# Optimization experiments

Measured on AMD Instinct MI355X. Metric: run time of the kernel, lower is better.

The kernel has to match this reference:

```python
import jax, jax.numpy as jnp
import numpy as np

C = 256      # MSA_channels
PC = 256     # pair_channels
G = 4        # groups
GP = C // G  # group_planes
FF = 4 * C
EPS = 1e-5


def layernorm(x, w, b):
    mu = jnp.mean(x, axis=-1, keepdims=True)
    var = jnp.mean(jnp.square(x - mu), axis=-1, keepdims=True)
    return (x - mu) * jax.lax.rsqrt(var + EPS) * w + b


def setup_inputs() -> dict:
    key = jax.random.key(0)
    ks = jax.random.split(key, 12)
    N, D, L = 1, 64, 512
    s = lambda fan_in: 1.0 / np.sqrt(fan_in)
    return {
        "msa_matrix": jax.random.normal(ks[0], (N, D, L, C), jnp.float32),
        "rr_edge": jax.random.normal(ks[1], (N, L, L, PC), jnp.float32),
        "ln_msa_w": jnp.ones((C,), jnp.float32),
        "ln_msa_b": jnp.zeros((C,), jnp.float32),
        "ln_rr_w": jnp.ones((PC,), jnp.float32),
        "ln_rr_b": jnp.zeros((PC,), jnp.float32),
        "WA": jax.random.normal(ks[2], (PC, G), jnp.float32) * s(PC),
        "bA": jnp.zeros((G,), jnp.float32),
        "WV": jax.random.normal(ks[3], (C, C), jnp.float32) * s(C),
        "bV": jnp.zeros((C,), jnp.float32),
        "WO": jax.random.normal(ks[4], (C, C), jnp.float32) * s(C),
        "bO": jnp.zeros((C,), jnp.float32),
        "ln_ff_w": jnp.ones((C,), jnp.float32),
        "ln_ff_b": jnp.zeros((C,), jnp.float32),
        "W1": jax.random.normal(ks[5], (C, FF), jnp.float32) * s(C),
        "b1": jnp.zeros((FF,), jnp.float32),
        "W2": jax.random.normal(ks[6], (FF, C), jnp.float32) * s(FF),
        "b2": jnp.zeros((C,), jnp.float32),
    }


def reference(msa_matrix, rr_edge, ln_msa_w, ln_msa_b, ln_rr_w, ln_rr_b,
              WA, bA, WV, bV, WO, bO, ln_ff_w, ln_ff_b, W1, b1, W2, b2):
    N, D, L, _ = msa_matrix.shape
    raw = msa_matrix
    m = layernorm(msa_matrix, ln_msa_w, ln_msa_b)          # [N,D,L,C]
    E = 0.5 * (rr_edge + jnp.swapaxes(rr_edge, 1, 2))      # symmetrize [N,L,L,PC]
    E = layernorm(E, ln_rr_w, ln_rr_b)
    A = jax.nn.softmax(E @ WA + bA, axis=2)                # [N,L,L,G], softmax over key dim j
    V = (m @ WV + bV).reshape(N, D, L, G, GP)              # [N,D,L,G,GP]
    agg = jnp.einsum('nijg,ndjgc->ndigc', A, V).reshape(N, D, L, C)
    out = agg @ WO + bO
    x = raw + out                                          # residual (dropout = identity at eval)
    h = layernorm(x, ln_ff_w, ln_ff_b)                     # FFN with pre-LN + residual
    return x + (jax.nn.relu(h @ W1 + b1) @ W2 + b2)
```

## Files before the change

### kernel.cpp

```cpp
#include <hip/hip_runtime.h>
#include <hip/hip_bf16.h>

typedef __bf16 bf16;
typedef bf16 bf16x8 __attribute__((ext_vector_type(8)));
typedef bf16 bf16x4v __attribute__((ext_vector_type(4)));
typedef float f32x4 __attribute__((ext_vector_type(4)));

#define LN_EPS 1e-5f

__device__ __forceinline__ void gload_lds16(const bf16* gsrc, bf16* ldst) {
  __builtin_amdgcn_global_load_lds(
      (const __attribute__((address_space(1))) void*)gsrc,
      (__attribute__((address_space(3))) void*)ldst, 16, 0, 0);
}

__global__ __launch_bounds__(256) void ln_rows_kernel(
    const float* __restrict__ in, const float* __restrict__ w,
    const float* __restrict__ b, bf16* __restrict__ out)
{
  int row = blockIdx.x * 4 + (threadIdx.x >> 6);
  int lane = threadIdx.x & 63;
  const float4* p = (const float4*)(in + (size_t)row * 256);
  float4 v = p[lane];
  float s = v.x + v.y + v.z + v.w;
  float q = v.x*v.x + v.y*v.y + v.z*v.z + v.w*v.w;
  #pragma unroll
  for (int o = 32; o; o >>= 1) { s += __shfl_xor(s, o); q += __shfl_xor(q, o); }
  float mu = s * (1.0f/256.0f);
  float rs = rsqrtf(q*(1.0f/256.0f) - mu*mu + LN_EPS);
  float4 wv = ((const float4*)w)[lane];
  float4 bv = ((const float4*)b)[lane];
  bf16x4v o4;
  o4[0] = (bf16)((v.x - mu)*rs*wv.x + bv.x);
  o4[1] = (bf16)((v.y - mu)*rs*wv.y + bv.y);
  o4[2] = (bf16)((v.z - mu)*rs*wv.z + bv.z);
  o4[3] = (bf16)((v.w - mu)*rs*wv.w + bv.w);
  *(bf16x4v*)(out + (size_t)row * 256 + lane * 4) = o4;
}

__global__ __launch_bounds__(256) void transpose_all_kernel(
    const float* __restrict__ WV, const float* __restrict__ WO,
    const float* __restrict__ W1, const float* __restrict__ W2,
    bf16* __restrict__ WVt, bf16* __restrict__ WOt,
    bf16* __restrict__ W1t, bf16* __restrict__ W2t)
{
  __shared__ float tile[32][33];
  int id = blockIdx.x;
  const float* in; bf16* out; int R, C, tpr;
  if (id < 64)       { in = WV; out = WVt; R = 256;  C = 256;  tpr = 8;  }
  else if (id < 128) { in = WO; out = WOt; R = 256;  C = 256;  tpr = 8;  id -= 64; }
  else if (id < 384) { in = W1; out = W1t; R = 256;  C = 1024; tpr = 32; id -= 128; }
  else               { in = W2; out = W2t; R = 1024; C = 256;  tpr = 8;  id -= 384; }
  int bc = (id % tpr) * 32, br = (id / tpr) * 32;
  int tx = threadIdx.x, ty = threadIdx.y;
  #pragma unroll
  for (int i = ty; i < 32; i += 8)
    tile[i][tx] = in[(size_t)(br + i) * C + bc + tx];
  __syncthreads();
  #pragma unroll
  for (int i = ty; i < 32; i += 8)
    out[(size_t)(bc + i) * R + br + tx] = (bf16)tile[tx][i];
}

__global__ __launch_bounds__(256) void sym_ln_wa_kernel(
    const float* __restrict__ rr, const float* __restrict__ w,
    const float* __restrict__ b, const float* __restrict__ WA,
    float* __restrict__ S)
{
  int rem = blockIdx.x; int ti = 0; int len = 32;
  while (rem >= len) { rem -= len; ti++; len--; }
  int tj = ti + rem;
  int wid = threadIdx.x >> 6, lane = threadIdx.x & 63;
  int c0 = lane * 4;
  float4 wv = ((const float4*)w)[lane];
  float4 bv = ((const float4*)b)[lane];
  const float4* wa4 = (const float4*)WA;
  float4 wa0 = wa4[c0+0], wa1 = wa4[c0+1], wa2 = wa4[c0+2], wa3 = wa4[c0+3];
  int pend = blockIdx.y * 64 + 64;
  for (int p = blockIdx.y * 64 + wid; p < pend; p += 4) {
    int i = ti*16 + (p >> 4), j = tj*16 + (p & 15);
    float4 a = ((const float4*)(rr + ((size_t)i*512 + j)*256))[lane];
    float4 c = ((const float4*)(rr + ((size_t)j*512 + i)*256))[lane];
    float ex = 0.5f*(a.x + c.x), ey = 0.5f*(a.y + c.y),
          ez = 0.5f*(a.z + c.z), ew = 0.5f*(a.w + c.w);
    float s = ex+ey+ez+ew;
    float q = ex*ex+ey*ey+ez*ez+ew*ew;
    #pragma unroll
    for (int o = 32; o; o >>= 1) { s += __shfl_xor(s, o); q += __shfl_xor(q, o); }
    float mu = s*(1.f/256.f);
    float rs = rsqrtf(q*(1.f/256.f) - mu*mu + LN_EPS);
    float nx = (ex-mu)*rs*wv.x + bv.x;
    float ny = (ey-mu)*rs*wv.y + bv.y;
    float nz = (ez-mu)*rs*wv.z + bv.z;
    float nw = (ew-mu)*rs*wv.w + bv.w;
    float g0 = nx*wa0.x + ny*wa1.x + nz*wa2.x + nw*wa3.x;
    float g1 = nx*wa0.y + ny*wa1.y + nz*wa2.y + nw*wa3.y;
    float g2 = nx*wa0.z + ny*wa1.z + nz*wa2.z + nw*wa3.z;
    float g3 = nx*wa0.w + ny*wa1.w + nz*wa2.w + nw*wa3.w;
    #pragma unroll
    for (int o = 32; o; o >>= 1) {
      g0 += __shfl_xor(g0, o); g1 += __shfl_xor(g1, o);
      g2 += __shfl_xor(g2, o); g3 += __shfl_xor(g3, o);
    }
    if (lane == 0) {
      float4 r4 = make_float4(g0, g1, g2, g3);
      ((float4*)S)[(size_t)i*512 + j] = r4;
      ((float4*)S)[(size_t)j*512 + i] = r4;
    }
  }
}

__global__ __launch_bounds__(256) void softmax_kernel(
    const float* __restrict__ S, bf16* __restrict__ Aout)
{
  int i = blockIdx.x * 4 + (threadIdx.x >> 6);
  int lane = threadIdx.x & 63;
  const float4* Sr = (const float4*)S + (size_t)i * 512;
  float4 s[8];
  float m0 = -1e30f, m1 = -1e30f, m2 = -1e30f, m3 = -1e30f;
  #pragma unroll
  for (int it = 0; it < 8; it++) {
    s[it] = Sr[lane + it*64];
    m0 = fmaxf(m0, s[it].x); m1 = fmaxf(m1, s[it].y);
    m2 = fmaxf(m2, s[it].z); m3 = fmaxf(m3, s[it].w);
  }
  #pragma unroll
  for (int o = 32; o; o >>= 1) {
    m0 = fmaxf(m0, __shfl_xor(m0, o)); m1 = fmaxf(m1, __shfl_xor(m1, o));
    m2 = fmaxf(m2, __shfl_xor(m2, o)); m3 = fmaxf(m3, __shfl_xor(m3, o));
  }
  float t0=0.f, t1=0.f, t2=0.f, t3=0.f;
  #pragma unroll
  for (int it = 0; it < 8; it++) {
    s[it].x = __expf(s[it].x - m0); t0 += s[it].x;
    s[it].y = __expf(s[it].y - m1); t1 += s[it].y;
    s[it].z = __expf(s[it].z - m2); t2 += s[it].z;
    s[it].w = __expf(s[it].w - m3); t3 += s[it].w;
  }
  #pragma unroll
  for (int o = 32; o; o >>= 1) {
    t0 += __shfl_xor(t0, o); t1 += __shfl_xor(t1, o);
    t2 += __shfl_xor(t2, o); t3 += __shfl_xor(t3, o);
  }
  t0 = 1.f/t0; t1 = 1.f/t1; t2 = 1.f/t2; t3 = 1.f/t3;
  bf16* A0 = Aout + (size_t)i * 512;
  #pragma unroll
  for (int it = 0; it < 8; it++) {
    int j = lane + it*64;
    A0[j]          = (bf16)(s[it].x * t0);
    A0[262144 + j] = (bf16)(s[it].y * t1);
    A0[524288 + j] = (bf16)(s[it].z * t2);
    A0[786432 + j] = (bf16)(s[it].w * t3);
  }
}

template<int MODE>
__global__ __launch_bounds__(256) void gemm_bt_kernel(
    const bf16* __restrict__ Aglob, const bf16* __restrict__ Bglob,
    void* __restrict__ outP, const float* __restrict__ bias,
    const float* __restrict__ resid, int M, int N, int K)
{
  __shared__ bf16 As[2][128 * 32];
  __shared__ bf16 Bs[2][128 * 32];
  int g = blockIdx.z;
  const bf16* Ag = Aglob;
  const bf16* Bg = Bglob;
  if (MODE == 1) { Ag += (size_t)g * 512 * 512; Bg += (size_t)g * 4096 * 512; }
  int bm = blockIdx.y * 128, bn = blockIdx.x * 128;
  int tid = threadIdx.x;
  int wid = tid >> 6, lane = tid & 63;
  int wm = (wid >> 1) * 64, wn = (wid & 1) * 64;
  f32x4 acc[4][4];
  #pragma unroll
  for (int mi = 0; mi < 4; mi++)
    #pragma unroll
    for (int ni = 0; ni < 4; ni++)
      acc[mi][ni] = (f32x4){0.f, 0.f, 0.f, 0.f};
  int c0 = wid * 2, c1 = wid * 2 + 1;
  int srow = lane >> 2;
  int scol = (lane & 3) * 8;
  const bf16* a0 = &Ag[(size_t)(bm + c0*16 + srow) * K + scol];
  const bf16* a1 = &Ag[(size_t)(bm + c1*16 + srow) * K + scol];
  const bf16* b0 = &Bg[(size_t)(bn + c0*16 + srow) * K + scol];
  const bf16* b1 = &Bg[(size_t)(bn + c1*16 + srow) * K + scol];
  int fr = lane & 15, fk = (lane >> 4) * 8;
  int nt = K >> 5;
  gload_lds16(a0, &As[0][c0 * 512]);
  gload_lds16(a1, &As[0][c1 * 512]);
  gload_lds16(b0, &Bs[0][c0 * 512]);
  gload_lds16(b1, &Bs[0][c1 * 512]);
  int cur = 0;
  for (int t = 0; t < nt; t++) {
    if (t + 1 < nt) {
      int k1 = (t + 1) << 5;
      gload_lds16(a0 + k1, &As[cur ^ 1][c0 * 512]);
      gload_lds16(a1 + k1, &As[cur ^ 1][c1 * 512]);
      gload_lds16(b0 + k1, &Bs[cur ^ 1][c0 * 512]);
      gload_lds16(b1 + k1, &Bs[cur ^ 1][c1 * 512]);
      asm volatile("s_waitcnt vmcnt(4)" ::: "memory");
    } else {
      asm volatile("s_waitcnt vmcnt(0)" ::: "memory");
    }
    __builtin_amdgcn_s_barrier();
    __builtin_amdgcn_sched_barrier(0);
    bf16x8 af[4], bf_[4];
    #pragma unroll
    for (int mi = 0; mi < 4; mi++) af[mi] = *(const bf16x8*)&As[cur][(wm + mi*16 + fr) * 32 + fk];
    #pragma unroll
    for (int ni = 0; ni < 4; ni++) bf_[ni] = *(const bf16x8*)&Bs[cur][(wn + ni*16 + fr) * 32 + fk];
    #pragma unroll
    for (int mi = 0; mi < 4; mi++)
      #pragma unroll
      for (int ni = 0; ni < 4; ni++)
        acc[mi][ni] = __builtin_amdgcn_mfma_f32_16x16x32_bf16(af[mi], bf_[ni], acc[mi][ni], 0, 0, 0);
    __builtin_amdgcn_sched_barrier(0);
    __builtin_amdgcn_s_barrier();
    cur ^= 1;
  }
  int cn0 = lane & 15;
  int rq = (lane >> 4) * 4;
  #pragma unroll
  for (int mi = 0; mi < 4; mi++) {
    #pragma unroll
    for (int ni = 0; ni < 4; ni++) {
      int mb = bm + wm + mi*16 + rq;
      int nc = bn + wn + ni*16 + cn0;
      #pragma unroll
      for (int r = 0; r < 4; r++) {
        int mr = mb + r;
        float v = acc[mi][ni][r];
        if (MODE == 0) {
          v += bias[mr];
          int gg = mr >> 6, rp = mr & 63, d = nc >> 9, j = nc & 511;
          ((bf16*)outP)[((size_t)gg*4096 + d*64 + rp)*512 + j] = (bf16)v;
        } else if (MODE == 1) {
          int d = nc >> 6, c6 = nc & 63;
          ((bf16*)outP)[((size_t)d*512 + mr)*256 + g*64 + c6] = (bf16)v;
        } else {
          v += bias[nc] + resid[(size_t)mr * N + nc];
          ((float*)outP)[(size_t)mr * N + nc] = v;
        }
      }
    }
  }
}

__global__ __launch_bounds__(256) void ffn_fused_kernel(
    const float* __restrict__ x, const float* __restrict__ lnw,
    const float* __restrict__ lnb, const bf16* __restrict__ W1t,
    const float* __restrict__ b1, const bf16* __restrict__ W2t,
    const float* __restrict__ b2, float* __restrict__ out)
{
  __shared__ __align__(16) char hbuf[64 * 512];
  __shared__ __align__(16) char tbuf[64 * 512];
  int tid = threadIdx.x;
  int wid = tid >> 6, lane = tid & 63;
  size_t row0 = (size_t)blockIdx.x * 64;

  {
    float4 wv = ((const float4*)lnw)[lane];
    float4 bv = ((const float4*)lnb)[lane];
    #pragma unroll 4
    for (int it = 0; it < 16; it++) {
      int row = wid * 16 + it;
      float4 v = ((const float4*)(x + (row0 + row) * 256))[lane];
      float s = v.x+v.y+v.z+v.w, q = v.x*v.x+v.y*v.y+v.z*v.z+v.w*v.w;
      #pragma unroll
      for (int o = 32; o; o >>= 1) { s += __shfl_xor(s, o); q += __shfl_xor(q, o); }
      float mu = s * (1.f/256.f);
      float rs = rsqrtf(q*(1.f/256.f) - mu*mu + LN_EPS);
      bf16x4v o4;
      o4[0] = (bf16)((v.x-mu)*rs*wv.x + bv.x);
      o4[1] = (bf16)((v.y-mu)*rs*wv.y + bv.y);
      o4[2] = (bf16)((v.z-mu)*rs*wv.z + bv.z);
      o4[3] = (bf16)((v.w-mu)*rs*wv.w + bv.w);
      *(bf16x4v*)(hbuf + row*512 + ((lane*8) ^ ((row & 7) << 4))) = o4;
    }
  }
  __syncthreads();

  int wn = wid * 64;
  int fr = lane & 15;
  int fk = (lane >> 4) * 8;
  int fk2 = fk * 2;
  int cn0 = lane & 15, rq = (lane >> 4) * 4;
  int arow[4], asw[4], brow[4];
  #pragma unroll
  for (int mi = 0; mi < 4; mi++) {
    arow[mi] = mi*16 + fr;
    asw[mi]  = (arow[mi] & 7) << 4;
  }
  #pragma unroll
  for (int ni = 0; ni < 4; ni++) brow[ni] = wn + ni*16 + fr;

  f32x4 acc2[4][4];
  #pragma unroll
  for (int mi = 0; mi < 4; mi++)
    #pragma unroll
    for (int ni = 0; ni < 4; ni++)
      acc2[mi][ni] = (f32x4){0.f, 0.f, 0.f, 0.f};

  for (int cf = 0; cf < 4; cf++) {
    f32x4 acc1[4][4];
    #pragma unroll
    for (int mi = 0; mi < 4; mi++)
      #pragma unroll
      for (int ni = 0; ni < 4; ni++)
        acc1[mi][ni] = (f32x4){0.f, 0.f, 0.f, 0.f};
    #pragma unroll 2
    for (int k0 = 0; k0 < 256; k0 += 32) {
      bf16x8 af[4], bf_[4];
      #pragma unroll
      for (int ni = 0; ni < 4; ni++)
        bf_[ni] = *(const bf16x8*)&W1t[(size_t)(cf*256 + brow[ni]) * 256 + k0 + fk];
      #pragma unroll
      for (int mi = 0; mi < 4; mi++)
        af[mi] = *(const bf16x8*)(hbuf + arow[mi]*512 + ((k0*2 + fk2) ^ asw[mi]));
      #pragma unroll
      for (int mi = 0; mi < 4; mi++)
        #pragma unroll
        for (int ni = 0; ni < 4; ni++)
          acc1[mi][ni] = __builtin_amdgcn_mfma_f32_16x16x32_bf16(af[mi], bf_[ni], acc1[mi][ni], 0, 0, 0);
    }
    __syncthreads();
    #pragma unroll
    for (int ni = 0; ni < 4; ni++) {
      int col = wn + ni*16 + cn0;
      float bb = b1[cf*256 + col];
      #pragma unroll
      for (int mi = 0; mi < 4; mi++) {
        #pragma unroll
        for (int r = 0; r < 4; r++) {
          int row = mi*16 + rq + r;
          float v = fmaxf(acc1[mi][ni][r] + bb, 0.f);
          *(bf16*)(tbuf + row*512 + ((col*2) ^ ((row & 7) << 4))) = (bf16)v;
        }
      }
    }
    __syncthreads();
    #pragma unroll 2
    for (int k0 = 0; k0 < 256; k0 += 32) {
      bf16x8 af[4], bf_[4];
      #pragma unroll
      for (int ni = 0; ni < 4; ni++)
        bf_[ni] = *(const bf16x8*)&W2t[(size_t)brow[ni] * 1024 + cf*256 + k0 + fk];
      #pragma unroll
      for (int mi = 0; mi < 4; mi++)
        af[mi] = *(const bf16x8*)(tbuf + arow[mi]*512 + ((k0*2 + fk2) ^ asw[mi]));
      #pragma unroll
      for (int mi = 0; mi < 4; mi++)
        #pragma unroll
        for (int ni = 0; ni < 4; ni++)
          acc2[mi][ni] = __builtin_amdgcn_mfma_f32_16x16x32_bf16(af[mi], bf_[ni], acc2[mi][ni], 0, 0, 0);
    }
  }
  #pragma unroll
  for (int ni = 0; ni < 4; ni++) {
    int col = wn + ni*16 + cn0;
    float bb = b2[col];
    #pragma unroll
    for (int mi = 0; mi < 4; mi++) {
      #pragma unroll
      for (int r = 0; r < 4; r++) {
        size_t grow = row0 + mi*16 + rq + r;
        out[grow*256 + col] = x[grow*256 + col] + acc2[mi][ni][r] + bb;
      }
    }
  }
}

extern "C" void kernel_launch(void* const* d_in, const int* in_sizes, int n_in,
                              void* d_out, int out_size, void* d_ws, size_t ws_size,
                              hipStream_t stream)
{
  (void)in_sizes; (void)n_in; (void)out_size; (void)ws_size;
  const float* msa = (const float*)d_in[0];
  const float* rr  = (const float*)d_in[1];
  const float* lmw = (const float*)d_in[2];
  const float* lmb = (const float*)d_in[3];
  const float* lrw = (const float*)d_in[4];
  const float* lrb = (const float*)d_in[5];
  const float* WA  = (const float*)d_in[6];
  const float* WV  = (const float*)d_in[8];
  const float* bV  = (const float*)d_in[9];
  const float* WO  = (const float*)d_in[10];
  const float* bO  = (const float*)d_in[11];
  const float* lfw = (const float*)d_in[12];
  const float* lfb = (const float*)d_in[13];
  const float* W1  = (const float*)d_in[14];
  const float* b1  = (const float*)d_in[15];
  const float* W2  = (const float*)d_in[16];
  const float* b2  = (const float*)d_in[17];
  float* out = (float*)d_out;
  char* ws = (char*)d_ws;
  float* S    = (float*)(ws + 0);
  bf16* Abuf  = (bf16*)(ws + 4194304);
  bf16* m     = (bf16*)(ws + 6291456);
  bf16* Vt    = (bf16*)(ws + 23068672);
  bf16* agg   = (bf16*)(ws + 39845888);
  bf16* WVt   = (bf16*)(ws + 83886080);
  bf16* WOt   = WVt + 65536;
  bf16* W1t   = WOt + 65536;
  bf16* W2t   = W1t + 262144;

  transpose_all_kernel<<<640, dim3(32, 8), 0, stream>>>(WV, WO, W1, W2, WVt, WOt, W1t, W2t);

  ln_rows_kernel<<<8192, 256, 0, stream>>>(msa, lmw, lmb, m);
  sym_ln_wa_kernel<<<dim3(528, 4), 256, 0, stream>>>(rr, lrw, lrb, WA, S);
  gemm_bt_kernel<0><<<dim3(256, 2, 1), 256, 0, stream>>>(WVt, m, Vt, bV, nullptr, 256, 32768, 256);
  softmax_kernel<<<128, 256, 0, stream>>>(S, Abuf);
  gemm_bt_kernel<1><<<dim3(32, 4, 4), 256, 0, stream>>>(Abuf, Vt, agg, nullptr, nullptr, 512, 4096, 512);
  gemm_bt_kernel<2><<<dim3(2, 256, 1), 256, 0, stream>>>(agg, WOt, out, bO, msa, 32768, 256, 256);
  ffn_fused_kernel<<<512, 256, 0, stream>>>(out, lfw, lfb, W1t, b1, W2t, b2, out);
}
```

Baseline: 263.0 us.

## Split fused FFN into LN+GEMM1 kernel and separate GEMM2 via workspace

Replaces the single fused FFN kernel, which kept the hidden activation in LDS and read weights straight from global memory, with two kernels. The first does the layernorm plus the first matmul with ReLU on 128x128 tiles, double-buffering W1 in LDS through direct global-to-LDS loads, and writes the bf16 hidden tensor to workspace. The existing tiled GEMM then computes the second matmul with bias and residual. This is meant to raise MFMA utilisation and weight reuse, at the cost of a 64 MB hidden-tensor round trip through HBM. Each first-stage block also recomputes the layernorm for its rows, so it is repeated once per column tile.

```diff
diff --git a/kernel.cpp b/kernel.cpp
--- a/kernel.cpp
+++ b/kernel.cpp
@@ -245,25 +245,23 @@
   }
 }
 
-__global__ __launch_bounds__(256) void ffn_fused_kernel(
+__global__ __launch_bounds__(256) void ffn1_kernel(
     const float* __restrict__ x, const float* __restrict__ lnw,
     const float* __restrict__ lnb, const bf16* __restrict__ W1t,
-    const float* __restrict__ b1, const bf16* __restrict__ W2t,
-    const float* __restrict__ b2, float* __restrict__ out)
-{
-  __shared__ __align__(16) char hbuf[64 * 512];
-  __shared__ __align__(16) char tbuf[64 * 512];
+    const float* __restrict__ b1, bf16* __restrict__ tout)
+{
+  __shared__ __align__(16) char hbuf[128 * 512];
+  __shared__ bf16 Bs[2][128 * 32];
   int tid = threadIdx.x;
   int wid = tid >> 6, lane = tid & 63;
-  size_t row0 = (size_t)blockIdx.x * 64;
+  int bm = blockIdx.y * 128, bn = blockIdx.x * 128;
 
   {
     float4 wv = ((const float4*)lnw)[lane];
     float4 bv = ((const float4*)lnb)[lane];
-    #pragma unroll 4
-    for (int it = 0; it < 16; it++) {
-      int row = wid * 16 + it;
-      float4 v = ((const float4*)(x + (row0 + row) * 256))[lane];
+    for (int it = 0; it < 32; it++) {
+      int row = wid * 32 + it;
+      float4 v = ((const float4*)(x + (size_t)(bm + row) * 256))[lane];
       float s = v.x+v.y+v.z+v.w, q = v.x*v.x+v.y*v.y+v.z*v.z+v.w*v.w;
       #pragma unroll
       for (int o = 32; o; o >>= 1) { s += __shfl_xor(s, o); q += __shfl_xor(q, o); }
@@ -279,91 +277,70 @@
   }
   __syncthreads();
 
-  int wn = wid * 64;
-  int fr = lane & 15;
-  int fk = (lane >> 4) * 8;
-  int fk2 = fk * 2;
-  int cn0 = lane & 15, rq = (lane >> 4) * 4;
-  int arow[4], asw[4], brow[4];
+  int wm = (wid >> 1) * 64, wn = (wid & 1) * 64;
+  int fr = lane & 15, fk = (lane >> 4) * 8, fk2 = fk * 2;
+  int arow[4], asw[4];
   #pragma unroll
   for (int mi = 0; mi < 4; mi++) {
-    arow[mi] = mi*16 + fr;
+    arow[mi] = wm + mi*16 + fr;
     asw[mi]  = (arow[mi] & 7) << 4;
   }
-  #pragma unroll
-  for (int ni = 0; ni < 4; ni++) brow[ni] = wn + ni*16 + fr;
-
-  f32x4 acc2[4][4];
+  f32x4 acc[4][4];
   #pragma unroll
   for (int mi = 0; mi < 4; mi++)
     #pragma unroll
     for (int ni = 0; ni < 4; ni++)
-      acc2[mi][ni] = (f32x4){0.f, 0.f, 0.f, 0.f};
-
-  for (int cf = 0; cf < 4; cf++) {
-    f32x4 acc1[4][4];
+      acc[mi][ni] = (f32x4){0.f, 0.f, 0.f, 0.f};
+
+  int c0 = wid * 2, c1 = wid * 2 + 1;
+  int srow = lane >> 2;
+  int scol = (lane & 3) * 8;
+  const bf16* b0 = &W1t[(size_t)(bn + c0*16 + srow) * 256 + scol];
+  const bf16* b1p = &W1t[(size_t)(bn + c1*16 + srow) * 256 + scol];
+  gload_lds16(b0, &Bs[0][c0 * 512]);
+  gload_lds16(b1p, &Bs[0][c1 * 512]);
+  int cur = 0;
+  for (int t = 0; t < 8; t++) {
+    if (t < 7) {
+      int k1 = (t + 1) << 5;
+      gload_lds16(b0 + k1, &Bs[cur ^ 1][c0 * 512]);
+      gload_lds16(b1p + k1, &Bs[cur ^ 1][c1 * 512]);
+      asm volatile("s_waitcnt vmcnt(2)" ::: "memory");
+    } else {
+      asm volatile("s_waitcnt vmcnt(0)" ::: "memory");
+    }
+    __builtin_amdgcn_s_barrier();
+    __builtin_amdgcn_sched_barrier(0);
+    int k0 = t << 5;
+    bf16x8 af[4], bf_[4];
     #pragma unroll
     for (int mi = 0; mi < 4; mi++)
+      af[mi] = *(const bf16x8*)(hbuf + arow[mi]*512 + ((k0*2 + fk2) ^ asw[mi]));
+    #pragma unroll
+    for (int ni = 0; ni < 4; ni++)
+      bf_[ni] = *(const bf16x8*)&Bs[cur][(wn + ni*16 + fr) * 32 + fk];
+    #pragma unroll
+    for (int mi = 0; mi < 4; mi++)
       #pragma unroll
       for (int ni = 0; ni < 4; ni++)
-        acc1[mi][ni] = (f32x4){0.f, 0.f, 0.f, 0.f};
-    #pragma unroll 2
-    for (int k0 = 0; k0 < 256; k0 += 32) {
-      bf16x8 af[4], bf_[4];
-      #pragma unroll
-      for (int ni = 0; ni < 4; ni++)
-        bf_[ni] = *(const bf16x8*)&W1t[(size_t)(cf*256 + brow[ni]) * 256 + k0 + fk];
-      #pragma unroll
-      for (int mi = 0; mi < 4; mi++)
-        af[mi] = *(const bf16x8*)(hbuf + arow[mi]*512 + ((k0*2 + fk2) ^ asw[mi]));
-      #pragma unroll
-      for (int mi = 0; mi < 4; mi++)
-        #pragma unroll
-        for (int ni = 0; ni < 4; ni++)
-          acc1[mi][ni] = __builtin_amdgcn_mfma_f32_16x16x32_bf16(af[mi], bf_[ni], acc1[mi][ni], 0, 0, 0);
-    }
-    __syncthreads();
-    #pragma unroll
-    for (int ni = 0; ni < 4; ni++) {
-      int col = wn + ni*16 + cn0;
-      float bb = b1[cf*256 + col];
-      #pragma unroll
-      for (int mi = 0; mi < 4; mi++) {
-        #pragma unroll
-        for (int r = 0; r < 4; r++) {
-          int row = mi*16 + rq + r;
-          float v = fmaxf(acc1[mi][ni][r] + bb, 0.f);
-          *(bf16*)(tbuf + row*512 + ((col*2) ^ ((row & 7) << 4))) = (bf16)v;
-        }
-      }
-    }
-    __syncthreads();
-    #pragma unroll 2
-    for (int k0 = 0; k0 < 256; k0 += 32) {
-      bf16x8 af[4], bf_[4];
-      #pragma unroll
-      for (int ni = 0; ni < 4; ni++)
-        bf_[ni] = *(const bf16x8*)&W2t[(size_t)brow[ni] * 1024 + cf*256 + k0 + fk];
-      #pragma unroll
-      for (int mi = 0; mi < 4; mi++)
-        af[mi] = *(const bf16x8*)(tbuf + arow[mi]*512 + ((k0*2 + fk2) ^ asw[mi]));
-      #pragma unroll
-      for (int mi = 0; mi < 4; mi++)
-        #pragma unroll
-        for (int ni = 0; ni < 4; ni++)
-          acc2[mi][ni] = __builtin_amdgcn_mfma_f32_16x16x32_bf16(af[mi], bf_[ni], acc2[mi][ni], 0, 0, 0);
-    }
-  }
+        acc[mi][ni] = __builtin_amdgcn_mfma_f32_16x16x32_bf16(af[mi], bf_[ni], acc[mi][ni], 0, 0, 0);
+    __builtin_amdgcn_sched_barrier(0);
+    __builtin_amdgcn_s_barrier();
+    cur ^= 1;
+  }
+  int cn0 = lane & 15;
+  int rq = (lane >> 4) * 4;
   #pragma unroll
   for (int ni = 0; ni < 4; ni++) {
-    int col = wn + ni*16 + cn0;
-    float bb = b2[col];
+    int nc = bn + wn + ni*16 + cn0;
+    float bb = b1[nc];
     #pragma unroll
     for (int mi = 0; mi < 4; mi++) {
       #pragma unroll
       for (int r = 0; r < 4; r++) {
-        size_t grow = row0 + mi*16 + rq + r;
-        out[grow*256 + col] = x[grow*256 + col] + acc2[mi][ni][r] + bb;
+        int mr = bm + wm + mi*16 + rq + r;
+        float v = fmaxf(acc[mi][ni][r] + bb, 0.f);
+        tout[(size_t)mr * 1024 + nc] = (bf16)v;
       }
     }
   }
@@ -393,6 +370,7 @@
   const float* b2  = (const float*)d_in[17];
   float* out = (float*)d_out;
   char* ws = (char*)d_ws;
+  bf16* tbuf  = (bf16*)(ws + 0);
   float* S    = (float*)(ws + 0);
   bf16* Abuf  = (bf16*)(ws + 4194304);
   bf16* m     = (bf16*)(ws + 6291456);
@@ -411,5 +389,6 @@
   softmax_kernel<<<128, 256, 0, stream>>>(S, Abuf);
   gemm_bt_kernel<1><<<dim3(32, 4, 4), 256, 0, stream>>>(Abuf, Vt, agg, nullptr, nullptr, 512, 4096, 512);
   gemm_bt_kernel<2><<<dim3(2, 256, 1), 256, 0, stream>>>(agg, WOt, out, bO, msa, 32768, 256, 256);
-  ffn_fused_kernel<<<512, 256, 0, stream>>>(out, lfw, lfb, W1t, b1, W2t, b2, out);
-}
+  ffn1_kernel<<<dim3(8, 256), 256, 0, stream>>>(out, lfw, lfb, W1t, b1, tbuf);
+  gemm_bt_kernel<2><<<dim3(2, 256, 1), 256, 0, stream>>>(tbuf, W2t, out, b2, out, 32768, 256, 1024);
+}
```

Measured after the change: 278.9 us. +6.1%, slower.
